# Optimization experiments

Hardware: AMD Instinct MI355X
Metric: run time of the kernel (lower is better)

The kernel has to match this reference:

```python
import jax, jax.numpy as jnp
import numpy as np

N_NODES = 100000
N_EDGES = 1000000


def setup_inputs() -> dict:
    key = jax.random.key(0)
    ks = jax.random.split(key, 8)
    x = jax.random.normal(ks[0], (N_NODES, 58), dtype=jnp.float32)
    edge_index = jax.random.randint(ks[1], (2, N_EDGES), 0, N_NODES, dtype=jnp.int64)
    # Glorot-ish scaled weights
    W1 = jax.random.normal(ks[2], (58, 300), dtype=jnp.float32) * (1.0 / np.sqrt(58))
    b1 = jnp.zeros((300,), dtype=jnp.float32)
    W2 = jax.random.normal(ks[3], (300, 100), dtype=jnp.float32) * (1.0 / np.sqrt(300))
    b2 = jnp.zeros((100,), dtype=jnp.float32)
    W3 = jax.random.normal(ks[4], (100, 1), dtype=jnp.float32) * (1.0 / np.sqrt(100))
    b3 = jnp.zeros((1,), dtype=jnp.float32)
    return {"x": x, "edge_index": edge_index, "W1": W1, "b1": b1,
            "W2": W2, "b2": b2, "W3": W3, "b3": b3}


def _gcn_norm(edge_index, num_nodes):
    # add self-loops, then symmetric normalization D^-1/2 A D^-1/2 (PyG gcn_norm)
    ar = jnp.arange(num_nodes, dtype=edge_index.dtype)
    ei = jnp.concatenate([edge_index, jnp.stack([ar, ar])], axis=1)
    row, col = ei[0], ei[1]
    deg = jax.ops.segment_sum(jnp.ones(row.shape[0], dtype=jnp.float32), col,
                              num_segments=num_nodes)
    dis = jnp.where(deg > 0, jax.lax.rsqrt(jnp.maximum(deg, 1.0)), 0.0)
    norm = dis[row] * dis[col]  # [E]
    return row, col, norm


def _gcn_conv(x, W, b, row, col, norm, num_nodes):
    h = x @ W                                  # [N, F_out]
    msg = h[row] * norm[:, None]               # gather + per-edge scale
    agg = jax.ops.segment_sum(msg, col, num_segments=num_nodes)  # scatter-add
    return agg + b


def reference(x, edge_index, W1, b1, W2, b2, W3, b3):
    n = x.shape[0]
    row, col, norm = _gcn_norm(edge_index, n)
    # eval mode: F.dropout(training=False) is identity
    h = jax.nn.relu(_gcn_conv(x, W1, b1, row, col, norm, n))
    h = jax.nn.relu(_gcn_conv(h, W2, b2, row, col, norm, n))
    out = _gcn_conv(h, W3, b3, row, col, norm, n)
    return out
```

## Files before the change

### kernel.cpp

```cpp
#include <hip/hip_runtime.h>
#include <hip/hip_bf16.h>

typedef __hip_bfloat16 bf16;
typedef __attribute__((ext_vector_type(8))) short s8v;
typedef __attribute__((ext_vector_type(4))) float f4v;

#define CAP 40

template <int MODE>
__device__ __forceinline__ float ld_m(const void* p, long long i, int dynbf) {
    if (MODE == 0) return ((const float*)p)[i];
    if (MODE == 1) return __bfloat162float(((const bf16*)p)[i]);
    return dynbf ? __bfloat162float(((const bf16*)p)[i]) : ((const float*)p)[i];
}
template <int MODE>
__device__ __forceinline__ void st_m(void* p, long long i, float v, int dynbf) {
    if (MODE == 0) { ((float*)p)[i] = v; return; }
    if (MODE == 1) { ((bf16*)p)[i] = __float2bfloat16(v); return; }
    if (dynbf) ((bf16*)p)[i] = __float2bfloat16(v);
    else       ((float*)p)[i] = v;
}

__device__ __forceinline__ float relu_keepnan(float v) { return (v <= 0.f) ? 0.f : v; }
__device__ __forceinline__ int clampi(int v, int lo, int hi) {
    return v < lo ? lo : (v > hi ? hi : v);
}
__device__ __forceinline__ short f2bf_bits(float v) {
    bf16 h = __float2bfloat16(v);
    return *(short*)&h;
}
__device__ __forceinline__ float bflo(unsigned w) { return __uint_as_float(w << 16); }
__device__ __forceinline__ float bfhi(unsigned w) { return __uint_as_float(w & 0xffff0000u); }
__device__ __forceinline__ unsigned pack2(float a, float b) {
    return ((unsigned)(unsigned short)f2bf_bits(a)) | (((unsigned)(unsigned short)f2bf_bits(b)) << 16);
}

__global__ void k_init(int* __restrict__ cnt, int n,
                       const int* __restrict__ ei, const unsigned* __restrict__ xw,
                       int* __restrict__ flags) {
    int i = blockIdx.x * blockDim.x + threadIdx.x;
    int stride = gridDim.x * blockDim.x;
    for (int j = i; j < n; j += stride) cnt[j] = 0;
    if (blockIdx.x == 0 && threadIdx.x < 64) {
        int lane = threadIdx.x;
        int ov = (lane < 16) ? ei[2 * lane + 1] : 0;
        unsigned long long be = __ballot(ov != 0);
        int inb = 0;
        #pragma unroll
        for (int q = 0; q < 2; ++q) {
            unsigned w = xw[lane + 64 * q];
            int e = (w >> 7) & 0xFF;
            inb += (e >= 110 && e <= 131) ? 1 : 0;
        }
        #pragma unroll
        for (int o = 32; o; o >>= 1) inb += __shfl_down(inb, o, 64);
        if (lane == 0) {
            flags[0] = (be == 0ULL) ? 1 : 0;
            flags[1] = (inb >= 64) ? 1 : 0;
        }
    }
}

__global__ void k_fill_prep(const int* __restrict__ ei, int* __restrict__ cnt,
                            int* __restrict__ csr_row, int E, int n, int psz, int CH,
                            int cblocks,
                            const void* __restrict__ x, const void* __restrict__ W1,
                            const void* __restrict__ W2, ushort* __restrict__ xq,
                            short* __restrict__ W1t, short* __restrict__ W2t,
                            const int* __restrict__ flags) {
    if ((int)blockIdx.x < cblocks) {
        int c = blockIdx.x >> 3;
        int p = blockIdx.x & 7;
        bool i64 = flags[0] != 0;
        const int plo = p * psz;
        const unsigned pun = (unsigned)psz;
        int lo = c * CH;
        int hi = lo + CH; if (hi > E) hi = E;
        const bool alOK = i64 ? ((E & 1) == 0) : ((E & 3) == 0);
        const int* cb32 = ei + E;
        const int* cb64 = ei + 2LL * E;
        for (int e = lo + threadIdx.x * 4; e < hi; e += 1024) {
            int cols[4];
            int m = hi - e; if (m > 4) m = 4;
            if (m == 4 && alOK) {
                if (i64) {
                    uint4 cv0 = *(const uint4*)(cb64 + 2LL * e);
                    uint4 cv1 = *(const uint4*)(cb64 + 2LL * e + 4);
                    cols[0] = (int)cv0.x; cols[1] = (int)cv0.z;
                    cols[2] = (int)cv1.x; cols[3] = (int)cv1.z;
                } else {
                    uint4 cv = *(const uint4*)(cb32 + e);
                    cols[0] = (int)cv.x; cols[1] = (int)cv.y;
                    cols[2] = (int)cv.z; cols[3] = (int)cv.w;
                }
            } else {
                #pragma unroll
                for (int j = 0; j < 4; ++j)
                    cols[j] = (j < m) ? (i64 ? cb64[2LL * (e + j)] : cb32[e + j])
                                      : -1;
            }
            #pragma unroll
            for (int j = 0; j < 4; ++j) {
                if (j >= m) continue;
                int col = clampi(cols[j], 0, n - 1);
                if ((unsigned)(col - plo) >= pun) continue;
                int r = ei[i64 ? 2LL * (e + j) : (long long)(e + j)];
                r = clampi(r, 0, n - 1);
                int pos = atomicAdd(&cnt[col], 1);
                if (pos >= 0 && pos < CAP) csr_row[(long long)col * CAP + pos] = r;
            }
        }
        return;
    }
    int fbf = flags[1];
    long long idx = (long long)(blockIdx.x - cblocks) * blockDim.x + threadIdx.x;
    long long nx8 = (long long)n * 8;
    if (idx < nx8) {
        int i = (int)(idx >> 3), f8 = (int)(idx & 7);
        int f = f8 * 8;
        uint4 outw;
        if (f8 < 7) {
            if (fbf) {
                const uint* up = (const uint*)((const ushort*)x + (long long)i * 58 + f);
                outw.x = up[0]; outw.y = up[1]; outw.z = up[2]; outw.w = up[3];
            } else {
                const float* xp = (const float*)x + (long long)i * 58 + f;
                float2 v0 = *(const float2*)(xp + 0);
                float2 v1 = *(const float2*)(xp + 2);
                float2 v2 = *(const float2*)(xp + 4);
                float2 v3 = *(const float2*)(xp + 6);
                outw.x = pack2(v0.x, v0.y);
                outw.y = pack2(v1.x, v1.y);
                outw.z = pack2(v2.x, v2.y);
                outw.w = pack2(v3.x, v3.y);
            }
        } else {
            if (fbf) {
                const uint* up = (const uint*)((const ushort*)x + (long long)i * 58 + 56);
                outw.x = up[0];
            } else {
                const float* xp = (const float*)x + (long long)i * 58 + 56;
                outw.x = pack2(xp[0], xp[1]);
            }
            outw.y = 0u; outw.z = 0u; outw.w = 0u;
        }
        *(uint4*)&xq[(long long)i * 64 + f] = outw;
        return;
    }
    long long j = idx - nx8;
    if (j < 320 * 64) {
        int nn = (int)(j >> 6), k = (int)(j & 63);
        float v = (nn < 300 && k < 58) ? ld_m<2>(W1, (long long)k * 300 + nn, fbf) : 0.f;
        W1t[j] = f2bf_bits(v);
        return;
    }
    long long j2 = j - 320 * 64;
    if (j2 < 128 * 320) {
        int nn = (int)(j2 / 320), k = (int)(j2 - (long long)nn * 320);
        float v = (nn < 100 && k < 300) ? ld_m<2>(W2, (long long)k * 100 + nn, fbf) : 0.f;
        W2t[j2] = f2bf_bits(v);
    }
}

__global__ void k_dis(const int* __restrict__ cnt, float* __restrict__ dis, int n) {
    int i = blockIdx.x * blockDim.x + threadIdx.x;
    if (i < n) dis[i] = rsqrtf(fmaxf((float)(cnt[i] + 1), 1.0f));
}

template <int OPN>
__global__ void k_aggo_pre(const uint4* __restrict__ src, uint4* __restrict__ dst,
                           const int* __restrict__ cnt, const int* __restrict__ csr_row,
                           const float* __restrict__ dis, int n) {
    long long idx = (long long)blockIdx.x * blockDim.x + threadIdx.x;
    if (idx >= (long long)n * OPN) return;
    int i = (int)(idx / OPN);
    int o = (int)(idx - (long long)i * OPN);
    float di = dis[i];
    uint4 sw = src[(long long)i * OPN + o];
    float a[8];
    a[0] = bflo(sw.x) * di; a[1] = bfhi(sw.x) * di;
    a[2] = bflo(sw.y) * di; a[3] = bfhi(sw.y) * di;
    a[4] = bflo(sw.z) * di; a[5] = bfhi(sw.z) * di;
    a[6] = bflo(sw.w) * di; a[7] = bfhi(sw.w) * di;
    int deg = cnt[i]; deg = clampi(deg, 0, CAP);
    int e0 = i * CAP;
    int e1 = e0 + deg;
    int e = e0;
    for (; e + 8 <= e1; e += 8) {
        int r[8];
        uint4 w[8];
        float d[8];
        #pragma unroll
        for (int j = 0; j < 8; ++j) r[j] = clampi(csr_row[e + j], 0, n - 1);
        #pragma unroll
        for (int j = 0; j < 8; ++j) w[j] = src[(long long)r[j] * OPN + o];
        #pragma unroll
        for (int j = 0; j < 8; ++j) d[j] = dis[r[j]];
        #pragma unroll
        for (int j = 0; j < 8; ++j) {
            a[0] = fmaf(bflo(w[j].x), d[j], a[0]);
            a[1] = fmaf(bfhi(w[j].x), d[j], a[1]);
            a[2] = fmaf(bflo(w[j].y), d[j], a[2]);
            a[3] = fmaf(bfhi(w[j].y), d[j], a[3]);
            a[4] = fmaf(bflo(w[j].z), d[j], a[4]);
            a[5] = fmaf(bfhi(w[j].z), d[j], a[5]);
            a[6] = fmaf(bflo(w[j].w), d[j], a[6]);
            a[7] = fmaf(bfhi(w[j].w), d[j], a[7]);
        }
    }
    for (; e + 4 <= e1; e += 4) {
        int r[4];
        uint4 w[4];
        float d[4];
        #pragma unroll
        for (int j = 0; j < 4; ++j) r[j] = clampi(csr_row[e + j], 0, n - 1);
        #pragma unroll
        for (int j = 0; j < 4; ++j) w[j] = src[(long long)r[j] * OPN + o];
        #pragma unroll
        for (int j = 0; j < 4; ++j) d[j] = dis[r[j]];
        #pragma unroll
        for (int j = 0; j < 4; ++j) {
            a[0] = fmaf(bflo(w[j].x), d[j], a[0]);
            a[1] = fmaf(bfhi(w[j].x), d[j], a[1]);
            a[2] = fmaf(bflo(w[j].y), d[j], a[2]);
            a[3] = fmaf(bfhi(w[j].y), d[j], a[3]);
            a[4] = fmaf(bflo(w[j].z), d[j], a[4]);
            a[5] = fmaf(bfhi(w[j].z), d[j], a[5]);
            a[6] = fmaf(bflo(w[j].w), d[j], a[6]);
            a[7] = fmaf(bfhi(w[j].w), d[j], a[7]);
        }
    }
    for (; e < e1; ++e) {
        int r = clampi(csr_row[e], 0, n - 1);
        uint4 w = src[(long long)r * OPN + o];
        float d = dis[r];
        a[0] = fmaf(bflo(w.x), d, a[0]);
        a[1] = fmaf(bfhi(w.x), d, a[1]);
        a[2] = fmaf(bflo(w.y), d, a[2]);
        a[3] = fmaf(bfhi(w.y), d, a[3]);
        a[4] = fmaf(bflo(w.z), d, a[4]);
        a[5] = fmaf(bfhi(w.z), d, a[5]);
        a[6] = fmaf(bflo(w.w), d, a[6]);
        a[7] = fmaf(bfhi(w.w), d, a[7]);
    }
    uint4 outw;
    outw.x = pack2(di * a[0], di * a[1]);
    outw.y = pack2(di * a[2], di * a[3]);
    outw.z = pack2(di * a[4], di * a[5]);
    outw.w = pack2(di * a[6], di * a[7]);
    dst[(long long)i * OPN + o] = outw;
}

__global__ void k_aggq_fused(const uint2* __restrict__ src, float* __restrict__ t3,
                             const int* __restrict__ cnt, const int* __restrict__ csr_row,
                             const float* __restrict__ dis, const void* __restrict__ b2,
                             const void* __restrict__ W3, int n,
                             const int* __restrict__ flags) {
    int tid = threadIdx.x;
    int ln = tid >> 5;
    int q  = tid & 31;
    int node = blockIdx.x * 8 + ln;
    if (node >= n) return;
    int fbf = flags[1];
    float di = dis[node];
    uint2 sw = src[(long long)node * 32 + q];
    float a0 = bflo(sw.x), a1 = bfhi(sw.x), a2 = bflo(sw.y), a3 = bfhi(sw.y);
    int deg = cnt[node]; deg = clampi(deg, 0, CAP);
    int e0 = node * CAP;
    int e1 = e0 + deg;
    int e = e0;
    for (; e + 8 <= e1; e += 8) {
        int r[8];
        uint2 w[8];
        #pragma unroll
        for (int j = 0; j < 8; ++j) r[j] = clampi(csr_row[e + j], 0, n - 1);
        #pragma unroll
        for (int j = 0; j < 8; ++j) w[j] = src[(long long)r[j] * 32 + q];
        #pragma unroll
        for (int j = 0; j < 8; ++j) {
            a0 += bflo(w[j].x); a1 += bfhi(w[j].x);
            a2 += bflo(w[j].y); a3 += bfhi(w[j].y);
        }
    }
    for (; e + 4 <= e1; e += 4) {
        int r[4];
        uint2 w[4];
        #pragma unroll
        for (int j = 0; j < 4; ++j) r[j] = clampi(csr_row[e + j], 0, n - 1);
        #pragma unroll
        for (int j = 0; j < 4; ++j) w[j] = src[(long long)r[j] * 32 + q];
        #pragma unroll
        for (int j = 0; j < 4; ++j) {
            a0 += bflo(w[j].x); a1 += bfhi(w[j].x);
            a2 += bflo(w[j].y); a3 += bfhi(w[j].y);
        }
    }
    for (; e < e1; ++e) {
        int r = clampi(csr_row[e], 0, n - 1);
        uint2 w = src[(long long)r * 32 + q];
        a0 += bflo(w.x); a1 += bfhi(w.x); a2 += bflo(w.y); a3 += bfhi(w.y);
    }
    int base = q * 4;
    float partial = 0.f;
    if (base < 100) {
        float o0 = relu_keepnan(di * a0 + ld_m<2>(b2, base + 0, fbf));
        float o1 = relu_keepnan(di * a1 + ld_m<2>(b2, base + 1, fbf));
        float o2 = relu_keepnan(di * a2 + ld_m<2>(b2, base + 2, fbf));
        float o3 = relu_keepnan(di * a3 + ld_m<2>(b2, base + 3, fbf));
        partial = o0 * ld_m<2>(W3, base + 0, fbf) + o1 * ld_m<2>(W3, base + 1, fbf)
                + o2 * ld_m<2>(W3, base + 2, fbf) + o3 * ld_m<2>(W3, base + 3, fbf);
    }
    partial += __shfl_xor(partial, 16, 64);
    partial += __shfl_xor(partial, 8, 64);
    partial += __shfl_xor(partial, 4, 64);
    partial += __shfl_xor(partial, 2, 64);
    partial += __shfl_xor(partial, 1, 64);
    if (q == 0) t3[node] = di * partial;
}

__global__ void k_agg1(const float* __restrict__ src, void* __restrict__ dst,
                       const int* __restrict__ cnt, const int* __restrict__ csr_row,
                       const float* __restrict__ dis, const void* __restrict__ bias,
                       int n, const int* __restrict__ flags) {
    int i = blockIdx.x * blockDim.x + threadIdx.x;
    if (i >= n) return;
    int fbf = flags[1];
    float di = dis[i];
    float acc = src[i];
    int deg = cnt[i]; deg = clampi(deg, 0, CAP);
    int e0 = i * CAP;
    int e1 = e0 + deg;
    int e = e0;
    for (; e + 4 <= e1; e += 4) {
        int r0 = clampi(csr_row[e],     0, n - 1);
        int r1 = clampi(csr_row[e + 1], 0, n - 1);
        int r2 = clampi(csr_row[e + 2], 0, n - 1);
        int r3 = clampi(csr_row[e + 3], 0, n - 1);
        acc += src[r0] + src[r1] + src[r2] + src[r3];
    }
    for (; e < e1; ++e) {
        int r = clampi(csr_row[e], 0, n - 1);
        acc += src[r];
    }
    float out = di * acc + ld_m<2>(bias, 0, fbf);
    st_m<2>(dst, i, out, fbf);
}

template <int NT, bool SCALE_ROW, bool HAS_BIAS, bool RELU>
__global__ __launch_bounds__(256) void k_gemm_mfma(
    const ushort* __restrict__ A, const ushort* __restrict__ Bt,
    const void* __restrict__ bias, const float* __restrict__ dis,
    bf16* __restrict__ C, int M, int KP, int chunks, int ldc, int NBreal,
    const int* __restrict__ flags) {
    constexpr int BN = NT * 16;
    __shared__ __align__(16) ushort A_s[128][40];
    __shared__ __align__(16) ushort B_s[BN][40];
    const int t = threadIdx.x;
    const int lane = t & 63;
    const int w = t >> 6;
    const int bm = blockIdx.y * 128;
    const int bn = blockIdx.x * BN;
    const int fbf = flags[1];
    const int mrow = lane & 15;
    const int quad = lane >> 4;

    f4v acc[2][NT];
    #pragma unroll
    for (int a = 0; a < 2; a++)
        #pragma unroll
        for (int b = 0; b < NT; b++)
            #pragma unroll
            for (int r = 0; r < 4; r++) acc[a][b][r] = 0.f;

    for (int c = 0; c < chunks; ++c) {
        const int k0 = c * 32;
        #pragma unroll
        for (int r = 0; r < 2; ++r) {
            int u = t + r * 256;
            int row = u >> 2, kq = (u & 3) * 8;
            int grow = bm + row;
            uint4 v = make_uint4(0u, 0u, 0u, 0u);
            if (grow < M) v = *(const uint4*)(A + (size_t)grow * KP + k0 + kq);
            *(uint4*)&A_s[row][kq] = v;
        }
        for (int u = t; u < BN * 4; u += 256) {
            int row = u >> 2, kq = (u & 3) * 8;
            uint4 v = *(const uint4*)(Bt + (size_t)(bn + row) * KP + k0 + kq);
            *(uint4*)&B_s[row][kq] = v;
        }
        __syncthreads();
        s8v a0 = *(const s8v*)&A_s[w * 32 + mrow][quad * 8];
        s8v a1 = *(const s8v*)&A_s[w * 32 + 16 + mrow][quad * 8];
        #pragma unroll
        for (int nt = 0; nt < NT; ++nt) {
            s8v b = *(const s8v*)&B_s[nt * 16 + mrow][quad * 8];
            acc[0][nt] = __builtin_amdgcn_mfma_f32_16x16x32_bf16(a0, b, acc[0][nt], 0, 0, 0);
            acc[1][nt] = __builtin_amdgcn_mfma_f32_16x16x32_bf16(a1, b, acc[1][nt], 0, 0, 0);
        }
        __syncthreads();
    }
    float sc[2][4];
    #pragma unroll
    for (int mi = 0; mi < 2; ++mi)
        #pragma unroll
        for (int r = 0; r < 4; ++r) {
            int gm = bm + w * 32 + mi * 16 + quad * 4 + r;
            sc[mi][r] = (SCALE_ROW && gm < M) ? dis[gm] : 1.f;
        }
    #pragma unroll
    for (int nt = 0; nt < NT; ++nt) {
        int gn = bn + nt * 16 + mrow;
        if (gn >= ldc) continue;
        float bv = 0.f;
        if (HAS_BIAS) bv = (gn < NBreal) ? ld_m<2>(bias, gn, fbf) : 0.f;
        #pragma unroll
        for (int mi = 0; mi < 2; ++mi)
            #pragma unroll
            for (int r = 0; r < 4; ++r) {
                int gm = bm + w * 32 + mi * 16 + quad * 4 + r;
                if (gm >= M) continue;
                float v = acc[mi][nt][r] * sc[mi][r];
                if (HAS_BIAS) v += bv;
                if (RELU) v = relu_keepnan(v);
                C[(size_t)gm * ldc + gn] = __float2bfloat16(v);
            }
    }
}

extern "C" void kernel_launch(void* const* d_in, const int* in_sizes, int n_in,
                              void* d_out, int out_size, void* d_ws, size_t ws_size,
                              hipStream_t stream) {
    const void* x  = d_in[0];
    const int*  ei = (const int*)d_in[1];
    const void* W1 = d_in[2];
    const void* b1 = d_in[3];
    const void* W2 = d_in[4];
    const void* b2 = d_in[5];
    const void* W3 = d_in[6];
    const void* b3 = d_in[7];

    const int F0 = 58;
    const int N = in_sizes[0] / F0;
    const int E = in_sizes[1] / 2;
    const int gy = (N + 127) / 128;
    const int CH = 4096;
    const int NC = (E + CH - 1) / CH;
    const int psz = (N + 7) / 8;

    size_t off = 0;
    auto alloc = [&](size_t bytes) -> void* {
        void* p = (char*)d_ws + off;
        off = (off + bytes + 255) & ~(size_t)255;
        return p;
    };
    int*   flags   = (int*)alloc(256);
    int*   cnt     = (int*)alloc((size_t)N * 4);
    float* dis     = (float*)alloc((size_t)N * 4);
    int*   csr_row = (int*)alloc((size_t)N * CAP * 4);
    short* W1t     = (short*)alloc((size_t)320 * 64 * 2);
    short* W2t     = (short*)alloc((size_t)128 * 320 * 2);
    float* t3      = (float*)alloc((size_t)N * 4);
    void*  regA    = alloc((size_t)N * 128 * 2);
    ushort* z_bf = (ushort*)regA;
    bf16*   t2   = (bf16*)regA;
    void*  regB    = alloc((size_t)N * 320 * 2);
    ushort* xq = (ushort*)regB;
    bf16*   h1 = (bf16*)regB;

    k_init<<<1024, 256, 0, stream>>>(cnt, N, ei, (const unsigned*)x, flags);
    {
        int cblocks = NC * 8;
        long long ptot = (long long)N * 8 + 320 * 64 + 128 * 320;
        int pblocks = (int)((ptot + 255) / 256);
        k_fill_prep<<<cblocks + pblocks, 256, 0, stream>>>(
            ei, cnt, csr_row, E, N, psz, CH, cblocks, x, W1, W2, xq, W1t, W2t, flags);
    }
    k_dis<<<(N + 255) / 256, 256, 0, stream>>>(cnt, dis, N);

    k_aggo_pre<8><<<((long long)N * 8 + 255) / 256, 256, 0, stream>>>(
        (const uint4*)xq, (uint4*)z_bf, cnt, csr_row, dis, N);
    k_gemm_mfma<10, false, true, true><<<dim3(2, gy), 256, 0, stream>>>(
        z_bf, (const ushort*)W1t, b1, dis, h1, N, 64, 2, 320, 300, flags);

    k_gemm_mfma<8, true, false, false><<<dim3(1, gy), 256, 0, stream>>>(
        (const ushort*)h1, (const ushort*)W2t, nullptr, dis, t2, N, 320, 10, 128, 0, flags);
    k_aggq_fused<<<(N + 7) / 8, 256, 0, stream>>>(
        (const uint2*)t2, t3, cnt, csr_row, dis, b2, W3, N, flags);

    k_agg1<<<(N + 255) / 256, 256, 0, stream>>>(
        t3, d_out, cnt, csr_row, dis, b3, N, flags);
}
```

Baseline: 313.1 us.

## Fuse layer-1 and layer-2 GEMMs to keep hidden activations in LDS

```diff
diff --git a/kernel.cpp b/kernel.cpp
--- a/kernel.cpp
+++ b/kernel.cpp
@@ -346,58 +346,89 @@
     st_m<2>(dst, i, out, fbf);
 }
 
-template <int NT, bool SCALE_ROW, bool HAS_BIAS, bool RELU>
-__global__ __launch_bounds__(256) void k_gemm_mfma(
-    const ushort* __restrict__ A, const ushort* __restrict__ Bt,
-    const void* __restrict__ bias, const float* __restrict__ dis,
-    bf16* __restrict__ C, int M, int KP, int chunks, int ldc, int NBreal,
-    const int* __restrict__ flags) {
-    constexpr int BN = NT * 16;
-    __shared__ __align__(16) ushort A_s[128][40];
-    __shared__ __align__(16) ushort B_s[BN][40];
+__global__ __launch_bounds__(256) void k_gemm12_fused(
+    const ushort* __restrict__ z,
+    const ushort* __restrict__ W1t,
+    const ushort* __restrict__ W2t,
+    const void* __restrict__ b1, const float* __restrict__ dis,
+    bf16* __restrict__ t2, int M, const int* __restrict__ flags) {
+    __shared__ __align__(16) ushort B1_s[64][72];
+    __shared__ __align__(16) ushort B2_s[128][72];
+    __shared__ __align__(16) ushort H_s[128][72];
     const int t = threadIdx.x;
     const int lane = t & 63;
     const int w = t >> 6;
-    const int bm = blockIdx.y * 128;
-    const int bn = blockIdx.x * BN;
+    const int bm = blockIdx.x * 128;
     const int fbf = flags[1];
     const int mrow = lane & 15;
     const int quad = lane >> 4;
 
-    f4v acc[2][NT];
+    s8v az[2][2];
     #pragma unroll
-    for (int a = 0; a < 2; a++)
-        #pragma unroll
-        for (int b = 0; b < NT; b++)
-            #pragma unroll
-            for (int r = 0; r < 4; r++) acc[a][b][r] = 0.f;
-
-    for (int c = 0; c < chunks; ++c) {
-        const int k0 = c * 32;
+    for (int mi = 0; mi < 2; ++mi)
+        #pragma unroll
+        for (int c = 0; c < 2; ++c) {
+            int grow = bm + w * 32 + mi * 16 + mrow;
+            uint4 v = make_uint4(0u, 0u, 0u, 0u);
+            if (grow < M) v = *(const uint4*)(z + (size_t)grow * 64 + c * 32 + quad * 8);
+            az[mi][c] = *(s8v*)&v;
+        }
+
+    f4v acc2[2][8];
+    #pragma unroll
+    for (int mi = 0; mi < 2; ++mi)
+        #pragma unroll
+        for (int nt = 0; nt < 8; ++nt)
+            #pragma unroll
+            for (int r = 0; r < 4; ++r) acc2[mi][nt][r] = 0.f;
+
+    for (int g = 0; g < 5; ++g) {
+        if (g) __syncthreads();
         #pragma unroll
         for (int r = 0; r < 2; ++r) {
             int u = t + r * 256;
-            int row = u >> 2, kq = (u & 3) * 8;
-            int grow = bm + row;
-            uint4 v = make_uint4(0u, 0u, 0u, 0u);
-            if (grow < M) v = *(const uint4*)(A + (size_t)grow * KP + k0 + kq);
-            *(uint4*)&A_s[row][kq] = v;
-        }
-        for (int u = t; u < BN * 4; u += 256) {
-            int row = u >> 2, kq = (u & 3) * 8;
-            uint4 v = *(const uint4*)(Bt + (size_t)(bn + row) * KP + k0 + kq);
-            *(uint4*)&B_s[row][kq] = v;
+            int row = u >> 3, kq = (u & 7) * 8;
+            *(uint4*)&B1_s[row][kq] = *(const uint4*)(W1t + (size_t)(g * 64 + row) * 64 + kq);
+        }
+        #pragma unroll
+        for (int r = 0; r < 4; ++r) {
+            int u = t + r * 256;
+            int row = u >> 3, kq = (u & 7) * 8;
+            *(uint4*)&B2_s[row][kq] = *(const uint4*)(W2t + (size_t)row * 320 + g * 64 + kq);
         }
         __syncthreads();
-        s8v a0 = *(const s8v*)&A_s[w * 32 + mrow][quad * 8];
-        s8v a1 = *(const s8v*)&A_s[w * 32 + 16 + mrow][quad * 8];
-        #pragma unroll
-        for (int nt = 0; nt < NT; ++nt) {
-            s8v b = *(const s8v*)&B_s[nt * 16 + mrow][quad * 8];
-            acc[0][nt] = __builtin_amdgcn_mfma_f32_16x16x32_bf16(a0, b, acc[0][nt], 0, 0, 0);
-            acc[1][nt] = __builtin_amdgcn_mfma_f32_16x16x32_bf16(a1, b, acc[1][nt], 0, 0, 0);
-        }
-        __syncthreads();
+        #pragma unroll
+        for (int nt = 0; nt < 4; ++nt) {
+            f4v acc1[2];
+            #pragma unroll
+            for (int r = 0; r < 4; ++r) { acc1[0][r] = 0.f; acc1[1][r] = 0.f; }
+            #pragma unroll
+            for (int c = 0; c < 2; ++c) {
+                s8v b = *(const s8v*)&B1_s[nt * 16 + mrow][c * 32 + quad * 8];
+                acc1[0] = __builtin_amdgcn_mfma_f32_16x16x32_bf16(az[0][c], b, acc1[0], 0, 0, 0);
+                acc1[1] = __builtin_amdgcn_mfma_f32_16x16x32_bf16(az[1][c], b, acc1[1], 0, 0, 0);
+            }
+            int gcol = g * 64 + nt * 16 + mrow;
+            float bv = (gcol < 300) ? ld_m<2>(b1, gcol, fbf) : 0.f;
+            #pragma unroll
+            for (int mi = 0; mi < 2; ++mi)
+                #pragma unroll
+                for (int r = 0; r < 4; ++r) {
+                    float v = relu_keepnan(acc1[mi][r] + bv);
+                    H_s[w * 32 + mi * 16 + quad * 4 + r][nt * 16 + mrow] = (ushort)f2bf_bits(v);
+                }
+        }
+        #pragma unroll
+        for (int c = 0; c < 2; ++c) {
+            s8v h0 = *(const s8v*)&H_s[w * 32 + mrow][c * 32 + quad * 8];
+            s8v h1 = *(const s8v*)&H_s[w * 32 + 16 + mrow][c * 32 + quad * 8];
+            #pragma unroll
+            for (int nt = 0; nt < 8; ++nt) {
+                s8v b = *(const s8v*)&B2_s[nt * 16 + mrow][c * 32 + quad * 8];
+                acc2[0][nt] = __builtin_amdgcn_mfma_f32_16x16x32_bf16(h0, b, acc2[0][nt], 0, 0, 0);
+                acc2[1][nt] = __builtin_amdgcn_mfma_f32_16x16x32_bf16(h1, b, acc2[1][nt], 0, 0, 0);
+            }
+        }
     }
     float sc[2][4];
     #pragma unroll
@@ -405,27 +436,22 @@
         #pragma unroll
         for (int r = 0; r < 4; ++r) {
             int gm = bm + w * 32 + mi * 16 + quad * 4 + r;
-            sc[mi][r] = (SCALE_ROW && gm < M) ? dis[gm] : 1.f;
+            sc[mi][r] = (gm < M) ? dis[gm] : 1.f;
         }
     #pragma unroll
-    for (int nt = 0; nt < NT; ++nt) {
-        int gn = bn + nt * 16 + mrow;
-        if (gn >= ldc) continue;
-        float bv = 0.f;
-        if (HAS_BIAS) bv = (gn < NBreal) ? ld_m<2>(bias, gn, fbf) : 0.f;
+    for (int nt = 0; nt < 8; ++nt) {
+        int gn = nt * 16 + mrow;
         #pragma unroll
         for (int mi = 0; mi < 2; ++mi)
             #pragma unroll
             for (int r = 0; r < 4; ++r) {
                 int gm = bm + w * 32 + mi * 16 + quad * 4 + r;
                 if (gm >= M) continue;
-                float v = acc[mi][nt][r] * sc[mi][r];
-                if (HAS_BIAS) v += bv;
-                if (RELU) v = relu_keepnan(v);
-                C[(size_t)gm * ldc + gn] = __float2bfloat16(v);
-            }
-    }
-}
+                t2[(size_t)gm * 128 + gn] = __float2bfloat16(acc2[mi][nt][r] * sc[mi][r]);
+            }
+    }
+}
+
 
 extern "C" void kernel_launch(void* const* d_in, const int* in_sizes, int n_in,
                               void* d_out, int out_size, void* d_ws, size_t ws_size,
@@ -460,12 +486,9 @@
     short* W1t     = (short*)alloc((size_t)320 * 64 * 2);
     short* W2t     = (short*)alloc((size_t)128 * 320 * 2);
     float* t3      = (float*)alloc((size_t)N * 4);
-    void*  regA    = alloc((size_t)N * 128 * 2);
-    ushort* z_bf = (ushort*)regA;
-    bf16*   t2   = (bf16*)regA;
-    void*  regB    = alloc((size_t)N * 320 * 2);
-    ushort* xq = (ushort*)regB;
-    bf16*   h1 = (bf16*)regB;
+    ushort* xq     = (ushort*)alloc((size_t)N * 64 * 2);
+    ushort* z_bf   = (ushort*)alloc((size_t)N * 64 * 2);
+    bf16*   t2     = (bf16*)alloc((size_t)N * 128 * 2);
 
     k_init<<<1024, 256, 0, stream>>>(cnt, N, ei, (const unsigned*)x, flags);
     {
@@ -479,11 +502,10 @@
 
     k_aggo_pre<8><<<((long long)N * 8 + 255) / 256, 256, 0, stream>>>(
         (const uint4*)xq, (uint4*)z_bf, cnt, csr_row, dis, N);
-    k_gemm_mfma<10, false, true, true><<<dim3(2, gy), 256, 0, stream>>>(
-        z_bf, (const ushort*)W1t, b1, dis, h1, N, 64, 2, 320, 300, flags);
-
-    k_gemm_mfma<8, true, false, false><<<dim3(1, gy), 256, 0, stream>>>(
-        (const ushort*)h1, (const ushort*)W2t, nullptr, dis, t2, N, 320, 10, 128, 0, flags);
+
+    k_gemm12_fused<<<gy, 256, 0, stream>>>(
+        z_bf, (const ushort*)W1t, (const ushort*)W2t, b1, dis, t2, N, flags);
+
     k_aggq_fused<<<(N + 7) / 8, 256, 0, stream>>>(
         (const uint2*)t2, t3, cnt, csr_row, dis, b2, W3, N, flags);
 
```

After: 263.5 us. 15.8% less time.
